# Kernel tuning notes

Measured on AMD Instinct MI355X. Metric: run time of the kernel, lower is better.

## Reference

```python
import jax, jax.numpy as jnp
import numpy as np

PAD_IDX = 1  # matches init_kwargs pad_idx
TLEN, BATCH, D_IN = 50, 16, 512
SRC_LEN, VOCAB, CVOCAB = 200, 20000, 20400


def setup_inputs() -> dict:
    key = jax.random.key(0)
    k1, k2, k3, k4, k5, k6, k7 = jax.random.split(key, 7)
    hidden = jax.random.normal(k1, (TLEN, BATCH, D_IN), dtype=jnp.float32)
    attn = jax.random.uniform(k2, (TLEN, BATCH, SRC_LEN), dtype=jnp.float32)
    # src_map is a sparse one-hot indicator: each source position maps to one extended-vocab id
    src_ids = jax.random.randint(k3, (SRC_LEN, BATCH), 0, CVOCAB)
    src_map = jax.nn.one_hot(src_ids, CVOCAB, dtype=jnp.float32)  # (src_len, batch, cvocab)
    s = 1.0 / np.sqrt(D_IN)
    W = jax.random.uniform(k4, (VOCAB, D_IN), dtype=jnp.float32, minval=-s, maxval=s)
    b = jax.random.uniform(k5, (VOCAB,), dtype=jnp.float32, minval=-s, maxval=s)
    Wc = jax.random.uniform(k6, (1, D_IN), dtype=jnp.float32, minval=-s, maxval=s)
    bc = jax.random.uniform(k7, (1,), dtype=jnp.float32, minval=-s, maxval=s)
    return {"hidden": hidden, "attn": attn, "src_map": src_map, "W": W, "b": b, "Wc": Wc, "bc": bc}


def reference(hidden, attn, src_map, W, b, Wc, bc):
    tlen, batch, _ = hidden.shape
    src_len, _, cvocab = src_map.shape
    logits = jnp.einsum('tbd,vd->tbv', hidden, W) + b            # (tlen, batch, vocab)
    # faithful to torch: logits[:, pad_idx] = -inf (indexes the batch dim!)
    logits = logits.at[:, PAD_IDX, :].set(-jnp.inf)
    prob = jax.nn.softmax(logits, axis=1)                        # softmax over dim 1, as in source
    p_copy = jax.nn.sigmoid(jnp.einsum('tbd,od->tbo', hidden, Wc) + bc)  # (tlen, batch, 1)
    out_prob = prob * (1.0 - p_copy)                             # (tlen, batch, vocab)
    mul_attn = attn * p_copy                                     # (tlen, batch, src_len)
    # bmm over batch with one-hot src_map: effectively a scatter-add into extended vocab
    copy_prob = jnp.einsum('tbs,sbv->tbv', mul_attn, src_map)    # (tlen, batch, cvocab)
    # faithful to the split/stack/transpose permutation in the source
    flat = copy_prob.reshape(tlen * batch, cvocab)
    copy_prob = flat.reshape(batch, tlen, cvocab).swapaxes(0, 1) # (tlen, batch, cvocab)
    copy_prob = copy_prob.at[:, :, :out_prob.shape[2]].add(out_prob)
    return copy_prob
```

## Files before the change

### kernel.cpp

```cpp
#include <hip/hip_runtime.h>
#include <cstdint>
#include <cstddef>

#define TLEN    50
#define BATCH   16
#define D_IN    512
#define SRC_LEN 200
#define VOCAB   20000
#define CVOCAB  20400

typedef __bf16 bf16x8 __attribute__((ext_vector_type(8)));
typedef float  f32x4  __attribute__((ext_vector_type(4)));

#define GEMM_BLOCKS 625
#define ZERO_BLOCKS 40
#define SCAN_BLOCKS (SRC_LEN * BATCH)
#define NT 128
#define APAD 8

__global__ __launch_bounds__(256)
void pc_kernel(const float* __restrict__ hidden,
               const float* __restrict__ Wc,
               const float* __restrict__ bc,
               float* __restrict__ pc)
{
    const int row  = blockIdx.x * 4 + (threadIdx.x >> 6);
    const int lane = threadIdx.x & 63;
    const float* h = hidden + (size_t)row * D_IN + lane * 8;
    float4 h0 = *(const float4*)(h);
    float4 h1 = *(const float4*)(h + 4);
    float4 w0 = *(const float4*)(Wc + lane * 8);
    float4 w1 = *(const float4*)(Wc + lane * 8 + 4);
    float s = h0.x*w0.x + h0.y*w0.y + h0.z*w0.z + h0.w*w0.w
            + h1.x*w1.x + h1.y*w1.y + h1.z*w1.z + h1.w*w1.w;
    #pragma unroll
    for (int o = 1; o < 64; o <<= 1) s += __shfl_xor(s, o);
    if (lane == 0) pc[row] = 1.0f / (1.0f + __expf(-(s + bc[0])));
}

__global__ __launch_bounds__(NT)
void fused_main(const float* __restrict__ hidden,
                const float* __restrict__ src_map,
                const float* __restrict__ W,
                const float* __restrict__ pc,
                float* __restrict__ out,
                int* __restrict__ src_ids)
{
    const int bid = blockIdx.x;
    const int tid = threadIdx.x;

    if (bid < GEMM_BLOCKS) {
        __shared__ __bf16 Alds[2][BATCH][D_IN + APAD];

        const int lane = tid & 63;
        const int wv   = tid >> 6;
        const int l15  = lane & 15;
        const int q    = lane >> 4;
        const int colbase = bid * 32 + wv * 16;

        bf16x8 bfrag[16];
        {
            const float* wrow = W + (size_t)(colbase + l15) * D_IN + q * 8;
            #pragma unroll
            for (int c = 0; c < 16; ++c) {
                float4 f0 = *(const float4*)(wrow + c * 32);
                float4 f1 = *(const float4*)(wrow + c * 32 + 4);
                bf16x8 bf;
                bf[0] = (__bf16)f0.x; bf[1] = (__bf16)f0.y;
                bf[2] = (__bf16)f0.z; bf[3] = (__bf16)f0.w;
                bf[4] = (__bf16)f1.x; bf[5] = (__bf16)f1.y;
                bf[6] = (__bf16)f1.z; bf[7] = (__bf16)f1.w;
                bfrag[c] = bf;
            }
            #pragma unroll
            for (int c = 0; c < 16; ++c) {
                f32x4 t = *(f32x4*)&bfrag[c];
                asm volatile("" : "+v"(t));
                bfrag[c] = *(bf16x8*)&t;
            }
        }

        auto stage = [&](int t, int buf) {
            #pragma unroll
            for (int i = 0; i < 16; ++i) {
                float4 v4 = *(const float4*)(hidden + ((size_t)t * BATCH + i) * D_IN + tid * 4);
                __bf16* dst = &Alds[buf][i][tid * 4];
                dst[0] = (__bf16)v4.x; dst[1] = (__bf16)v4.y;
                dst[2] = (__bf16)v4.z; dst[3] = (__bf16)v4.w;
            }
        };

        stage(0, 0);

        for (int t = 0; t < TLEN; ++t) {
            __syncthreads();
            if (t + 1 < TLEN) stage(t + 1, (t + 1) & 1);

            const __bf16* arow = &Alds[t & 1][l15][q * 8];
            f32x4 accA = {0.f, 0.f, 0.f, 0.f};
            f32x4 accB = {0.f, 0.f, 0.f, 0.f};
            #pragma unroll
            for (int c = 0; c < 16; c += 2) {
                bf16x8 a0 = *(const bf16x8*)(arow + c * 32);
                bf16x8 a1 = *(const bf16x8*)(arow + c * 32 + 32);
                accA = __builtin_amdgcn_mfma_f32_16x16x32_bf16(a0, bfrag[c],     accA, 0, 0, 0);
                accB = __builtin_amdgcn_mfma_f32_16x16x32_bf16(a1, bfrag[c + 1], accB, 0, 0, 0);
            }
            f32x4 acc = accA + accB;

            float4 pc4 = *(const float4*)(pc + t * 16 + q * 4);

            float mx = -INFINITY;
            #pragma unroll
            for (int r = 0; r < 4; ++r)
                if (q * 4 + r != 1) mx = fmaxf(mx, acc[r]);
            mx = fmaxf(mx, __shfl_xor(mx, 16));
            mx = fmaxf(mx, __shfl_xor(mx, 32));
            float e[4], s = 0.f;
            #pragma unroll
            for (int r = 0; r < 4; ++r) {
                e[r] = (q * 4 + r == 1) ? 0.f : __expf(acc[r] - mx);
                s += e[r];
            }
            s += __shfl_xor(s, 16);
            s += __shfl_xor(s, 32);
            const float inv = 1.0f / s;
            const int v = colbase + l15;
            #pragma unroll
            for (int r = 0; r < 4; ++r) {
                const int b = q * 4 + r;
                out[(size_t)(t * BATCH + b) * CVOCAB + v] = e[r] * inv * (1.0f - pc4[r]);
            }
        }
    } else if (bid < GEMM_BLOCKS + ZERO_BLOCKS) {
        const int zb = bid - GEMM_BLOCKS;
        const float4 z = {0.f, 0.f, 0.f, 0.f};
        for (int i = tid; i < 2000; i += NT) {
            const int f = zb * 2000 + i;
            const int r = f / 100;
            const int c = f % 100;
            *(float4*)(out + (size_t)r * CVOCAB + VOCAB + c * 4) = z;
        }
    } else {
        const int row = bid - GEMM_BLOCKS - ZERO_BLOCKS;
        const float4* base = (const float4*)(src_map + (size_t)row * CVOCAB);
        int found = -1;
        for (int i0 = tid; i0 < 1275; i0 += NT) {
            float4 x0 = base[i0];
            float4 x1 = base[i0 + 1275];
            float4 x2 = base[i0 + 2550];
            float4 x3 = base[i0 + 3825];
            #pragma unroll
            for (int seg = 0; seg < 4; ++seg) {
                float4 x = seg == 0 ? x0 : seg == 1 ? x1 : seg == 2 ? x2 : x3;
                const int e0 = (i0 + seg * 1275) * 4;
                if (x.x > 0.5f) found = e0;
                if (x.y > 0.5f) found = e0 + 1;
                if (x.z > 0.5f) found = e0 + 2;
                if (x.w > 0.5f) found = e0 + 3;
            }
        }
        if (found >= 0) src_ids[row] = found;
    }
}

__global__ __launch_bounds__(256)
void scatter_copy(const float* __restrict__ attn,
                  const float* __restrict__ pc,
                  const int* __restrict__ src_ids,
                  float* __restrict__ out)
{
    const int p  = blockIdx.x;
    const int si = threadIdx.x;
    if (si >= SRC_LEN) return;
    const int b  = p & 15;
    const size_t obase = (size_t)((p % TLEN) * BATCH + (p / TLEN)) * CVOCAB;
    const int id = src_ids[si * BATCH + b];
    const float val = attn[(size_t)p * SRC_LEN + si] * pc[p];
    if ((unsigned)id < (unsigned)CVOCAB)
        atomicAdd(out + obase + id, val);
}

extern "C" void kernel_launch(void* const* d_in, const int* in_sizes, int n_in,
                              void* d_out, int out_size, void* d_ws, size_t ws_size,
                              hipStream_t stream)
{
    const float* hidden  = (const float*)d_in[0];
    const float* attn    = (const float*)d_in[1];
    const float* src_map = (const float*)d_in[2];
    const float* W       = (const float*)d_in[3];
    const float* Wc      = (const float*)d_in[5];
    const float* bc      = (const float*)d_in[6];
    float* out   = (float*)d_out;
    int* src_ids = (int*)d_ws;
    float* pc    = (float*)d_ws + 3200;

    pc_kernel<<<dim3(200), dim3(256), 0, stream>>>(hidden, Wc, bc, pc);
    fused_main<<<dim3(GEMM_BLOCKS + ZERO_BLOCKS + SCAN_BLOCKS), dim3(NT), 0, stream>>>(
        hidden, src_map, W, pc, out, src_ids);
    scatter_copy<<<dim3(TLEN * BATCH), dim3(256), 0, stream>>>(attn, pc, src_ids, out);
}
```

Before: 438.4 us.

## Pre-convert hidden to bf16 once and read MFMA A-fragments directly from global

The pc kernel now also writes a bf16 copy of hidden to workspace. The GEMM blocks then load their A fragments straight from that buffer instead of staging fp32 hidden into double-buffered LDS with barriers. This drops the per-block fp32 loads and conversions, the LDS traffic and the __syncthreads. In exchange every wave issues its own global and L2 reads of A each timestep, and those reads are no longer overlapped with compute by explicit prefetching.

```diff
diff --git a/kernel.cpp b/kernel.cpp
--- a/kernel.cpp
+++ b/kernel.cpp
@@ -16,19 +16,26 @@
 #define ZERO_BLOCKS 40
 #define SCAN_BLOCKS (SRC_LEN * BATCH)
 #define NT 128
-#define APAD 8
 
 __global__ __launch_bounds__(256)
 void pc_kernel(const float* __restrict__ hidden,
                const float* __restrict__ Wc,
                const float* __restrict__ bc,
-               float* __restrict__ pc)
+               float* __restrict__ pc,
+               __bf16* __restrict__ hbf)
 {
     const int row  = blockIdx.x * 4 + (threadIdx.x >> 6);
     const int lane = threadIdx.x & 63;
     const float* h = hidden + (size_t)row * D_IN + lane * 8;
     float4 h0 = *(const float4*)(h);
     float4 h1 = *(const float4*)(h + 4);
+    bf16x8 hb;
+    hb[0] = (__bf16)h0.x; hb[1] = (__bf16)h0.y;
+    hb[2] = (__bf16)h0.z; hb[3] = (__bf16)h0.w;
+    hb[4] = (__bf16)h1.x; hb[5] = (__bf16)h1.y;
+    hb[6] = (__bf16)h1.z; hb[7] = (__bf16)h1.w;
+    *(bf16x8*)(hbf + (size_t)row * D_IN + lane * 8) = hb;
+
     float4 w0 = *(const float4*)(Wc + lane * 8);
     float4 w1 = *(const float4*)(Wc + lane * 8 + 4);
     float s = h0.x*w0.x + h0.y*w0.y + h0.z*w0.z + h0.w*w0.w
@@ -39,7 +46,7 @@
 }
 
 __global__ __launch_bounds__(NT)
-void fused_main(const float* __restrict__ hidden,
+void fused_main(const __bf16* __restrict__ hbf,
                 const float* __restrict__ src_map,
                 const float* __restrict__ W,
                 const float* __restrict__ pc,
@@ -50,8 +57,6 @@
     const int tid = threadIdx.x;
 
     if (bid < GEMM_BLOCKS) {
-        __shared__ __bf16 Alds[2][BATCH][D_IN + APAD];
-
         const int lane = tid & 63;
         const int wv   = tid >> 6;
         const int l15  = lane & 15;
@@ -80,23 +85,8 @@
             }
         }
 
-        auto stage = [&](int t, int buf) {
-            #pragma unroll
-            for (int i = 0; i < 16; ++i) {
-                float4 v4 = *(const float4*)(hidden + ((size_t)t * BATCH + i) * D_IN + tid * 4);
-                __bf16* dst = &Alds[buf][i][tid * 4];
-                dst[0] = (__bf16)v4.x; dst[1] = (__bf16)v4.y;
-                dst[2] = (__bf16)v4.z; dst[3] = (__bf16)v4.w;
-            }
-        };
-
-        stage(0, 0);
-
         for (int t = 0; t < TLEN; ++t) {
-            __syncthreads();
-            if (t + 1 < TLEN) stage(t + 1, (t + 1) & 1);
-
-            const __bf16* arow = &Alds[t & 1][l15][q * 8];
+            const __bf16* arow = hbf + ((size_t)t * BATCH + l15) * D_IN + q * 8;
             f32x4 accA = {0.f, 0.f, 0.f, 0.f};
             f32x4 accB = {0.f, 0.f, 0.f, 0.f};
             #pragma unroll
@@ -192,11 +182,13 @@
     const float* Wc      = (const float*)d_in[5];
     const float* bc      = (const float*)d_in[6];
     float* out   = (float*)d_out;
-    int* src_ids = (int*)d_ws;
-    float* pc    = (float*)d_ws + 3200;
 
-    pc_kernel<<<dim3(200), dim3(256), 0, stream>>>(hidden, Wc, bc, pc);
+    int*    src_ids = (int*)d_ws;
+    float*  pc      = (float*)((char*)d_ws + 12800);
+    __bf16* hbf     = (__bf16*)((char*)d_ws + 16000);
+
+    pc_kernel<<<dim3(200), dim3(256), 0, stream>>>(hidden, Wc, bc, pc, hbf);
     fused_main<<<dim3(GEMM_BLOCKS + ZERO_BLOCKS + SCAN_BLOCKS), dim3(NT), 0, stream>>>(
-        hidden, src_map, W, pc, out, src_ids);
+        hbf, src_map, W, pc, out, src_ids);
     scatter_copy<<<dim3(TLEN * BATCH), dim3(256), 0, stream>>>(attn, pc, src_ids, out);
 }
```

New measurement: 524.0 us. 1.2x slower.
